# Kernel optimization log

Hardware: AMD Instinct MI355X
Metric: run time of the kernel (lower is better)

The kernel has to match this reference:

```python
import jax, jax.numpy as jnp
import numpy as np

N_NODES = 50000
N_EDGES = 800000
IN_F = 128
HID = 256
N_CLS = 10
NUM_GRAPHS = 256


def setup_inputs() -> dict:
    key = jax.random.key(0)
    ks = jax.random.split(key, 8)
    x = jax.random.normal(ks[0], (N_NODES, IN_F), dtype=jnp.float32)
    edge_index = jax.random.randint(ks[1], (2, N_EDGES), 0, N_NODES, dtype=jnp.int64)
    batch = jnp.sort(jax.random.randint(ks[2], (N_NODES,), 0, NUM_GRAPHS, dtype=jnp.int64))
    # Glorot-style init for weights (GCNConv default), zeros bias
    W1 = jax.random.normal(ks[3], (IN_F, HID), dtype=jnp.float32) / np.sqrt(IN_F)
    b1 = jnp.zeros((HID,), dtype=jnp.float32)
    W2 = jax.random.normal(ks[4], (HID, HID), dtype=jnp.float32) / np.sqrt(HID)
    b2 = jnp.zeros((HID,), dtype=jnp.float32)
    Wlin = jax.random.normal(ks[5], (HID, N_CLS), dtype=jnp.float32) / np.sqrt(HID)
    blin = jnp.zeros((N_CLS,), dtype=jnp.float32)
    return {"x": x, "edge_index": edge_index, "batch": batch,
            "W1": W1, "b1": b1, "W2": W2, "b2": b2, "Wlin": Wlin, "blin": blin}


def reference(x, edge_index, batch, W1, b1, W2, b2, Wlin, blin):
    N = x.shape[0]
    # PyG GCNConv default: add self-loops, symmetric normalization D^-1/2 A D^-1/2
    loop = jnp.arange(N, dtype=edge_index.dtype)
    src = jnp.concatenate([edge_index[0], loop])  # message source (row)
    dst = jnp.concatenate([edge_index[1], loop])  # aggregation target (col)
    deg = jax.ops.segment_sum(jnp.ones_like(dst, dtype=x.dtype), dst, num_segments=N)
    dinv = jnp.where(deg > 0, jax.lax.rsqrt(deg), 0.0)
    norm = dinv[src] * dinv[dst]  # [E+N]

    def gcn_conv(h, W, b):
        h = h @ W                          # linear transform first (GCNConv)
        msg = h[src] * norm[:, None]       # gather + edge scale
        agg = jax.ops.segment_sum(msg, dst, num_segments=N)  # scatter-add
        return agg + b

    h = jax.nn.relu(gcn_conv(x, W1, b1))
    h = gcn_conv(h, W2, b2)

    # global_mean_pool over batch ids
    counts = jax.ops.segment_sum(jnp.ones((N,), x.dtype), batch, num_segments=NUM_GRAPHS)
    pooled = jax.ops.segment_sum(h, batch, num_segments=NUM_GRAPHS)
    pooled = pooled / jnp.maximum(counts, 1.0)[:, None]  # [NUM_GRAPHS, HID]

    return pooled @ Wlin + blin  # forward returns logits (softmax unused in forward)
```

## Files before the change

kernel.cpp:

```cpp
#include <hip/hip_runtime.h>
#include <hip/hip_bf16.h>

typedef __hip_bfloat16 bf16;
typedef __attribute__((ext_vector_type(8))) short short8;
typedef __attribute__((ext_vector_type(4))) float f32x4;
typedef __attribute__((ext_vector_type(2))) float f32x2;

#define N_NODES 50000
#define N_EDGES 800000
#define IN_F    128
#define HID     256
#define N_CLS   10
#define N_GRAPH 256

#define NB 98
#define PBLOCKS 256

__device__ __forceinline__ int IG(const int* __restrict__ p, int i, int w) {
    return w ? p[2 * i] : p[i];
}
__device__ __forceinline__ float LF(const void* __restrict__ p, int i, int isbf) {
    return isbf ? __bfloat162float(((const bf16*)p)[i]) : ((const float*)p)[i];
}
__device__ __forceinline__ float b2f(unsigned short h) {
    union { unsigned u; float f; } c; c.u = ((unsigned)h) << 16; return c.f;
}
__device__ __forceinline__ unsigned short f2b(float x) {
    bf16 h = __float2bfloat16(x);
    union { bf16 b; unsigned short u; } c; c.b = h; return c.u;
}
__device__ __forceinline__ float f8s(unsigned b) {
    union { unsigned u; float f; } c;
    c.u = ((b & 0x80u) << 24) | ((b & 0x7Fu) << 20);
    return c.f;
}
#define F8SCALE 0x1p120f
__device__ __forceinline__ unsigned f2fp8(float x) {
    unsigned short h = f2b(x * 0x1p-120f);
    unsigned s = ((unsigned)h >> 8) & 0x80u;
    unsigned mag = (unsigned)h & 0x7FFFu;
    unsigned r = (mag + 7u + ((mag >> 4) & 1u)) >> 4;
    if (r > 0x7Eu) r = 0x7Eu;
    return s | r;
}

#if defined(__has_builtin)
#if __has_builtin(__builtin_amdgcn_cvt_pk_f32_fp8)
#define HW_FP8 1
#endif
#endif

__device__ __forceinline__ f32x2 cvt2lo(unsigned v) {
#ifdef HW_FP8
    return __builtin_amdgcn_cvt_pk_f32_fp8((int)v, false);
#else
    f32x2 r; r[0] = f8s(v & 0xFF) * F8SCALE; r[1] = f8s((v >> 8) & 0xFF) * F8SCALE; return r;
#endif
}
__device__ __forceinline__ f32x2 cvt2hi(unsigned v) {
#ifdef HW_FP8
    return __builtin_amdgcn_cvt_pk_f32_fp8((int)v, true);
#else
    f32x2 r; r[0] = f8s((v >> 16) & 0xFF) * F8SCALE; r[1] = f8s(v >> 24) * F8SCALE; return r;
#endif
}

__global__ __launch_bounds__(256) void k_detect(const int* __restrict__ ei,
                                                const unsigned short* __restrict__ x,
                                                int* __restrict__ flags) {
    __shared__ int nz, cnt;
    if (threadIdx.x == 0) { nz = 0; cnt = 0; }
    __syncthreads();
    int found = 0, c = 0;
    for (int s = 0; s < 4; ++s) {
        int idx = 2 * (threadIdx.x * 4 + s) + 1;
        if (ei[idx] != 0) found = 1;
    }
    for (int s = 0; s < 8; ++s) {
        unsigned short h = x[threadIdx.x * 8 + s];
        int e = (h >> 7) & 0xFF;
        if (e >= 110 && e <= 135) c++;
    }
    if (found) atomicAdd(&nz, 1);
    atomicAdd(&cnt, c);
    __syncthreads();
    if (threadIdx.x == 0) {
        flags[0] = (nz == 0) ? 1 : 0;
        flags[1] = (cnt > 1536) ? 1 : 0;
    }
}

__global__ __launch_bounds__(256) void k_partA1(const int* __restrict__ ei, int* __restrict__ bucketCnt,
                                                int* __restrict__ blockBase, const int* __restrict__ flags,
                                                int E, int N) {
    __shared__ int h[NB];
    int t = threadIdx.x;
    if (t < NB) h[t] = 0;
    __syncthreads();
    int w = flags[0];
    for (int e = blockIdx.x * 256 + t; e < E; e += PBLOCKS * 256) {
        int d = IG(ei, E + e, w);
        int s = IG(ei, e, w);
        if ((unsigned)d < (unsigned)N && (unsigned)s < (unsigned)N)
            atomicAdd(&h[d >> 9], 1);
    }
    __syncthreads();
    if (t < NB)
        blockBase[blockIdx.x * NB + t] = atomicAdd(&bucketCnt[t * 16], h[t]);
}

__global__ __launch_bounds__(128) void k_bscan(const int* __restrict__ bucketCnt,
                                               int* __restrict__ bucketBase) {
    __shared__ int s[128];
    int t = threadIdx.x;
    int v = (t < NB) ? bucketCnt[t * 16] : 0;
    s[t] = v;
    __syncthreads();
    for (int off = 1; off < 128; off <<= 1) {
        int add = (t >= off) ? s[t - off] : 0;
        __syncthreads();
        s[t] += add;
        __syncthreads();
    }
    if (t <= NB) bucketBase[t] = (t < NB) ? (s[t] - v) : s[NB - 1] + 0;
    if (t == NB - 1) bucketBase[NB] = s[t];
}

__global__ __launch_bounds__(256) void k_partA2(const int* __restrict__ ei,
                                                const int* __restrict__ bucketBase,
                                                const int* __restrict__ blockBase,
                                                unsigned* __restrict__ part,
                                                const int* __restrict__ flags, int E, int N) {
    __shared__ int cur[NB];
    int t = threadIdx.x;
    if (t < NB) cur[t] = bucketBase[t] + blockBase[blockIdx.x * NB + t];
    __syncthreads();
    int w = flags[0];
    for (int e = blockIdx.x * 256 + t; e < E; e += PBLOCKS * 256) {
        int d = IG(ei, E + e, w);
        int s = IG(ei, e, w);
        if ((unsigned)d < (unsigned)N && (unsigned)s < (unsigned)N) {
            int slot = atomicAdd(&cur[d >> 9], 1);
            part[slot] = ((unsigned)(d & 511) << 16) | (unsigned)s;
        }
    }
}

__global__ __launch_bounds__(256) void k_partB(const unsigned* __restrict__ part,
                                               const int* __restrict__ bucketBase,
                                               int* __restrict__ rowptr, float* __restrict__ dinv,
                                               int* __restrict__ col, int N) {
    __shared__ int hist[512];
    __shared__ int scn[512];
    __shared__ int pair[256];
    int b = blockIdx.x, t = threadIdx.x;
    int s0 = bucketBase[b], e0 = bucketBase[b + 1];
    hist[t] = 0; hist[t + 256] = 0;
    __syncthreads();
    for (int j = s0 + t; j < e0; j += 256)
        atomicAdd(&hist[part[j] >> 16], 1);
    __syncthreads();
    int a0 = hist[2 * t], a1 = hist[2 * t + 1];
    int pv = a0 + a1;
    pair[t] = pv;
    __syncthreads();
    for (int off = 1; off < 256; off <<= 1) {
        int add = (t >= off) ? pair[t - off] : 0;
        __syncthreads();
        pair[t] += add;
        __syncthreads();
    }
    int pbase = pair[t] - pv;
    scn[2 * t] = pbase;
    scn[2 * t + 1] = pbase + a0;
    __syncthreads();
#pragma unroll
    for (int hh = 0; hh < 2; ++hh) {
        int l = t + hh * 256;
        int node = b * 512 + l;
        if (node < N) {
            rowptr[node] = s0 + scn[l];
            dinv[node] = rsqrtf((float)(hist[l] + 1));
        }
    }
    if (b == 0 && t == 0) rowptr[N] = bucketBase[NB];
    __syncthreads();
    for (int j = s0 + t; j < e0; j += 256) {
        unsigned p = part[j];
        int pos = s0 + atomicAdd(&scn[p >> 16], 1);
        col[pos] = (int)(p & 0xFFFFu);
    }
}

#define CVTX_BLOCKS 6250
#define CVT1_BLOCKS 128
#define CVT2_BLOCKS 256
#define GB_BLOCKS   196
__global__ __launch_bounds__(256) void k_cvt(const void* __restrict__ x, const float* __restrict__ dinv,
                                             unsigned char* __restrict__ xs8,
                                             const void* __restrict__ W1, unsigned short* __restrict__ w1t,
                                             const void* __restrict__ W2, unsigned short* __restrict__ w2t,
                                             const int* __restrict__ batch, int* __restrict__ gstart,
                                             const int* __restrict__ flags) {
    int b = blockIdx.x;
    int fb = flags[1];
    if (b < CVTX_BLOCKS) {
        int gid = b * 256 + threadIdx.x;
        int row = gid >> 5;
        float d = dinv[row];
        float vx, vy, vz, vw;
        if (fb) {
            ushort4 v = ((const ushort4*)x)[gid];
            vx = b2f(v.x); vy = b2f(v.y); vz = b2f(v.z); vw = b2f(v.w);
        } else {
            float4 v = ((const float4*)x)[gid];
            vx = v.x; vy = v.y; vz = v.z; vw = v.w;
        }
        unsigned o = f2fp8(vx * d) | (f2fp8(vy * d) << 8) |
                     (f2fp8(vz * d) << 16) | (f2fp8(vw * d) << 24);
        ((unsigned*)xs8)[gid] = o;
    } else if (b < CVTX_BLOCKS + CVT1_BLOCKS) {
        int i = (b - CVTX_BLOCKS) * 256 + threadIdx.x;
        int n = i >> 7, k = i & 127;
        w1t[i] = f2b(LF(W1, k * 256 + n, fb));
    } else if (b < CVTX_BLOCKS + CVT1_BLOCKS + CVT2_BLOCKS) {
        int i = (b - CVTX_BLOCKS - CVT1_BLOCKS) * 256 + threadIdx.x;
        int n = i >> 8, k = i & 255;
        w2t[i] = f2b(LF(W2, k * 256 + n, fb));
    } else {
        int i = (b - CVTX_BLOCKS - CVT1_BLOCKS - CVT2_BLOCKS) * 256 + threadIdx.x;
        if (i <= N_NODES) {
            int w = flags[0];
            int prev = (i == 0) ? -1 : IG(batch, i - 1, w);
            int cur  = (i == N_NODES) ? N_GRAPH : IG(batch, i, w);
            if (prev < -1) prev = -1;
            if (cur > N_GRAPH) cur = N_GRAPH;
            for (int g = prev + 1; g <= cur; ++g)
                if (g >= 0 && g <= N_GRAPH) gstart[g] = i;
        }
    }
}

#define BSTR 132
__global__ __launch_bounds__(256) void k_gemm(const unsigned short* __restrict__ A,
                                              const unsigned short* __restrict__ Bt,
                                              unsigned short* __restrict__ C,
                                              unsigned char* __restrict__ C8, int M, int K,
                                              const float* __restrict__ rowscale,
                                              const void* __restrict__ bias,
                                              const int* __restrict__ flags, int relu) {
    __shared__ unsigned short Bs[128 * BSTR];
    int t = threadIdx.x;
    int lane = t & 63;
    int w = t >> 6;
    int stripe = blockIdx.y;
    int bm = blockIdx.x * 128;
    int l15 = lane & 15, quad = lane >> 4;
    const short8 Z8 = {0, 0, 0, 0, 0, 0, 0, 0};
    f32x4 acc[2][8];
#pragma unroll
    for (int i = 0; i < 2; ++i)
#pragma unroll
        for (int j = 0; j < 8; ++j) acc[i][j] = (f32x4){0.f, 0.f, 0.f, 0.f};

    int row0 = bm + w * 32 + l15;
    int row1 = row0 + 16;
    for (int kp = 0; kp < K; kp += 128) {
        if (kp) __syncthreads();
        {
            int n = t >> 1, h = t & 1;
            const unsigned short* src = &Bt[(size_t)(stripe * 128 + n) * K + kp + h * 64];
            unsigned short* dst = &Bs[n * BSTR + h * 64];
#pragma unroll
            for (int j = 0; j < 8; ++j)
                *(uint4*)&dst[j * 8] = *(const uint4*)&src[j * 8];
        }
        __syncthreads();
#pragma unroll
        for (int ks = 0; ks < 4; ++ks) {
            const unsigned short* abase = &A[(size_t)row0 * K + kp + ks * 32 + quad * 8];
            short8 a0 = (row0 < M) ? *(const short8*)abase : Z8;
            short8 a1 = (row1 < M) ? *(const short8*)(abase + (size_t)16 * K) : Z8;
#pragma unroll
            for (int tt = 0; tt < 8; ++tt) {
                short8 b = *(const short8*)&Bs[(tt * 16 + l15) * BSTR + ks * 32 + quad * 8];
                acc[0][tt] = __builtin_amdgcn_mfma_f32_16x16x32_bf16(b, a0, acc[0][tt], 0, 0, 0);
                acc[1][tt] = __builtin_amdgcn_mfma_f32_16x16x32_bf16(b, a1, acc[1][tt], 0, 0, 0);
            }
        }
    }
    int fb = flags[1];
    int rowA[2];
    float drow[2];
#pragma unroll
    for (int sa = 0; sa < 2; ++sa) {
        rowA[sa] = bm + w * 32 + sa * 16 + l15;
        drow[sa] = (rowscale && rowA[sa] < M) ? rowscale[rowA[sa]] : 1.f;
    }
#pragma unroll
    for (int tt = 0; tt < 8; ++tt) {
        int colb = stripe * 128 + tt * 16 + quad * 4;
        float bc[4];
#pragma unroll
        for (int rr = 0; rr < 4; ++rr)
            bc[rr] = bias ? LF(bias, colb + rr, fb) : 0.f;
#pragma unroll
        for (int sa = 0; sa < 2; ++sa) {
            if (rowA[sa] < M) {
                float v[4];
#pragma unroll
                for (int rr = 0; rr < 4; ++rr) {
                    float u = fmaf(acc[sa][tt][rr], drow[sa], bc[rr]);
                    if (relu) u = fmaxf(u, 0.f);
                    v[rr] = u;
                }
                size_t base = (size_t)rowA[sa] * 256 + colb;
                if (C8) {
                    unsigned o = f2fp8(v[0]) | (f2fp8(v[1]) << 8) |
                                 (f2fp8(v[2]) << 16) | (f2fp8(v[3]) << 24);
                    *(unsigned*)&C8[base] = o;
                } else {
                    ushort4 o;
                    o.x = f2b(v[0]); o.y = f2b(v[1]);
                    o.z = f2b(v[2]); o.w = f2b(v[3]);
                    *(ushort4*)&C[base] = o;
                }
            }
        }
    }
}

__global__ __launch_bounds__(256) void k_agg2(const unsigned char* __restrict__ XS,
                                              const int* __restrict__ rowptr, const int* __restrict__ col,
                                              unsigned short* __restrict__ Hout, int N) {
    int lane = threadIdx.x & 63;
    int i = (blockIdx.x * 256 + threadIdx.x) >> 6;
    if (i >= N) return;
    int fo = lane * 2;
    unsigned sv = *(const unsigned short*)&XS[(size_t)i * 128 + fo];
    f32x2 a = cvt2lo(sv);
    int s = rowptr[i], e = rowptr[i + 1];
    int j = s;
    while (j + 16 <= e) {
        unsigned v[16];
#pragma unroll
        for (int q = 0; q < 16; ++q)
            v[q] = *(const unsigned short*)&XS[(size_t)col[j + q] * 128 + fo];
#pragma unroll
        for (int q = 0; q < 16; ++q) a += cvt2lo(v[q]);
        j += 16;
    }
    if (j + 8 <= e) {
        unsigned v[8];
#pragma unroll
        for (int q = 0; q < 8; ++q)
            v[q] = *(const unsigned short*)&XS[(size_t)col[j + q] * 128 + fo];
#pragma unroll
        for (int q = 0; q < 8; ++q) a += cvt2lo(v[q]);
        j += 8;
    }
    if (j + 4 <= e) {
        unsigned v[4];
#pragma unroll
        for (int q = 0; q < 4; ++q)
            v[q] = *(const unsigned short*)&XS[(size_t)col[j + q] * 128 + fo];
#pragma unroll
        for (int q = 0; q < 4; ++q) a += cvt2lo(v[q]);
        j += 4;
    }
    for (; j < e; ++j)
        a += cvt2lo(*(const unsigned short*)&XS[(size_t)col[j] * 128 + fo]);
    ushort2 o;
    o.x = f2b(a[0]); o.y = f2b(a[1]);
    *(ushort2*)&Hout[(size_t)i * 128 + fo] = o;
}

__global__ __launch_bounds__(256) void k_agg4(const unsigned char* __restrict__ XW,
                                              const int* __restrict__ rowptr, const int* __restrict__ col,
                                              const float* __restrict__ dinv, const void* __restrict__ bias,
                                              const int* __restrict__ flags,
                                              unsigned short* __restrict__ Hout, int N) {
    int lane = threadIdx.x & 63;
    int i = (blockIdx.x * 256 + threadIdx.x) >> 6;
    if (i >= N) return;
    int fo = lane * 4;
    unsigned sv = *(const unsigned*)&XW[(size_t)i * 256 + fo];
    f32x2 a01 = cvt2lo(sv), a23 = cvt2hi(sv);
    int s = rowptr[i], e = rowptr[i + 1];
    int j = s;
    while (j + 16 <= e) {
        unsigned v[16];
#pragma unroll
        for (int q = 0; q < 16; ++q)
            v[q] = *(const unsigned*)&XW[(size_t)col[j + q] * 256 + fo];
#pragma unroll
        for (int q = 0; q < 16; ++q) { a01 += cvt2lo(v[q]); a23 += cvt2hi(v[q]); }
        j += 16;
    }
    if (j + 8 <= e) {
        unsigned v[8];
#pragma unroll
        for (int q = 0; q < 8; ++q)
            v[q] = *(const unsigned*)&XW[(size_t)col[j + q] * 256 + fo];
#pragma unroll
        for (int q = 0; q < 8; ++q) { a01 += cvt2lo(v[q]); a23 += cvt2hi(v[q]); }
        j += 8;
    }
    if (j + 4 <= e) {
        unsigned v[4];
#pragma unroll
        for (int q = 0; q < 4; ++q)
            v[q] = *(const unsigned*)&XW[(size_t)col[j + q] * 256 + fo];
#pragma unroll
        for (int q = 0; q < 4; ++q) { a01 += cvt2lo(v[q]); a23 += cvt2hi(v[q]); }
        j += 4;
    }
    for (; j < e; ++j) {
        unsigned v = *(const unsigned*)&XW[(size_t)col[j] * 256 + fo];
        a01 += cvt2lo(v); a23 += cvt2hi(v);
    }
    int fb = flags[1];
    float di = dinv[i];
    float bx = LF(bias, fo + 0, fb), by = LF(bias, fo + 1, fb);
    float bz = LF(bias, fo + 2, fb), bw = LF(bias, fo + 3, fb);
    ushort4 o;
    o.x = f2b(fmaf(a01[0], di, bx)); o.y = f2b(fmaf(a01[1], di, by));
    o.z = f2b(fmaf(a23[0], di, bz)); o.w = f2b(fmaf(a23[1], di, bw));
    *(ushort4*)&Hout[(size_t)i * 256 + fo] = o;
}

__global__ __launch_bounds__(256) void k_poolfinal(const unsigned short* __restrict__ H2,
                                                   const int* __restrict__ gstart,
                                                   const void* __restrict__ Wlin,
                                                   const void* __restrict__ blin,
                                                   const int* __restrict__ flags,
                                                   void* __restrict__ outv) {
    __shared__ float red[4][256];
    __shared__ float p[256];
    int g = blockIdx.x, t = threadIdx.x;
    int sub = t >> 6, lane = t & 63;
    int s = gstart[g], e = gstart[g + 1];
    int cnt = e - s;
    float ax = 0.f, ay = 0.f, az = 0.f, aw = 0.f;
    for (int i = s + sub; i < e; i += 4) {
        ushort4 v = *(const ushort4*)&H2[(size_t)i * 256 + lane * 4];
        ax += b2f(v.x); ay += b2f(v.y); az += b2f(v.z); aw += b2f(v.w);
    }
    red[sub][lane * 4 + 0] = ax;
    red[sub][lane * 4 + 1] = ay;
    red[sub][lane * 4 + 2] = az;
    red[sub][lane * 4 + 3] = aw;
    __syncthreads();
    float inv = 1.f / fmaxf((float)cnt, 1.f);
    p[t] = (red[0][t] + red[1][t] + red[2][t] + red[3][t]) * inv;
    __syncthreads();
    int fb = flags[1];
    if (t < N_CLS) {
        float sum = LF(blin, t, fb);
        for (int f = 0; f < HID; ++f) sum = fmaf(p[f], LF(Wlin, f * N_CLS + t, fb), sum);
        if (fb) ((bf16*)outv)[g * N_CLS + t] = __float2bfloat16(sum);
        else    ((float*)outv)[g * N_CLS + t] = sum;
    }
}

extern "C" void kernel_launch(void* const* d_in, const int* in_sizes, int n_in,
                              void* d_out, int out_size, void* d_ws, size_t ws_size,
                              hipStream_t stream) {
    (void)n_in; (void)ws_size; (void)in_sizes; (void)out_size;
    const void* x     = d_in[0];
    const int*  ei    = (const int*)d_in[1];
    const int*  batch = (const int*)d_in[2];
    const void* W1    = d_in[3];
    const void* b1    = d_in[4];
    const void* W2    = d_in[5];
    const void* b2    = d_in[6];
    const void* Wl    = d_in[7];
    const void* bl    = d_in[8];

    const int N = N_NODES, E = N_EDGES, F = IN_F, H = HID, G = N_GRAPH;

    char* ws = (char*)d_ws;
    size_t off = 0;
    auto alloc = [&](size_t bytes) -> void* {
        void* p = ws + off;
        off += (bytes + 511) & ~(size_t)511;
        return p;
    };
    unsigned char*  xs8  = (unsigned char*)alloc((size_t)N * F);
    unsigned short* aggX = (unsigned short*)alloc((size_t)N * F * 2);
    unsigned short* H1   = (unsigned short*)alloc((size_t)N * H * 2);
    unsigned short* H2   = (unsigned short*)alloc((size_t)N * H * 2);
    unsigned char*  XW2s8 = xs8;
    unsigned short* w1t  = (unsigned short*)alloc((size_t)H * F * 2);
    unsigned short* w2t  = (unsigned short*)alloc((size_t)H * H * 2);
    int*   bucketCnt = (int*)alloc((size_t)NB * 16 * 4);
    int*   bucketBase = (int*)alloc((size_t)(NB + 1) * 4);
    int*   blockBase = (int*)alloc((size_t)PBLOCKS * NB * 4);
    unsigned* part  = (unsigned*)alloc((size_t)E * 4);
    int*   gstart  = (int*)alloc((size_t)(G + 1) * 4);
    float* dinv    = (float*)alloc((size_t)N * 4);
    int*   rowptr  = (int*)alloc((size_t)(N + 1) * 4);
    int*   flags   = (int*)alloc(512);
    int*   col     = (int*)alloc((size_t)E * 4);
    size_t zero_bytes = (size_t)NB * 16 * 4;

    hipMemsetAsync(bucketCnt, 0, zero_bytes, stream);

    k_detect<<<1, 256, 0, stream>>>(ei, (const unsigned short*)x, flags);
    k_partA1<<<PBLOCKS, 256, 0, stream>>>(ei, bucketCnt, blockBase, flags, E, N);
    k_bscan<<<1, 128, 0, stream>>>(bucketCnt, bucketBase);
    k_partA2<<<PBLOCKS, 256, 0, stream>>>(ei, bucketBase, blockBase, part, flags, E, N);
    k_partB<<<NB, 256, 0, stream>>>(part, bucketBase, rowptr, dinv, col, N);

    k_cvt<<<CVTX_BLOCKS + CVT1_BLOCKS + CVT2_BLOCKS + GB_BLOCKS, 256, 0, stream>>>(
        x, dinv, xs8, W1, w1t, W2, w2t, batch, gstart, flags);

    dim3 gemmGrid((N + 127) / 128, 2);
    int nbAgg = (N + 3) / 4;

    k_agg2<<<nbAgg, 256, 0, stream>>>(xs8, rowptr, col, aggX, N);
    k_gemm<<<gemmGrid, 256, 0, stream>>>(aggX, w1t, H1, nullptr, N, F, dinv, b1, flags, 1);
    k_gemm<<<gemmGrid, 256, 0, stream>>>(H1, w2t, nullptr, XW2s8, N, H, dinv, nullptr, flags, 0);
    k_agg4<<<nbAgg, 256, 0, stream>>>(XW2s8, rowptr, col, dinv, b2, flags, H2, N);
    k_poolfinal<<<G, 256, 0, stream>>>(H2, gstart, Wl, bl, flags, d_out);
}
```

Before: 284.3 us.

## Stage GEMM epilogue through shared memory and use hardware fp8 pack conversion

The GEMM epilogue now writes bias/scale/relu results into the shared B tile, then each thread writes contiguous 64-byte or 128-byte row segments to global memory. Before, each lane made scattered 4-byte or 8-byte stores. The float-to-fp8 packing also switches to the hardware cvt_pk_fp8_f32 builtin when available, replacing the software rounding path. Together these aim to coalesce output writes and cut ALU work in the epilogue. The cost is extra syncthreads and LDS traffic, and the hardware fp8 format and scaling may not match the software encoding (which uses a 2^-120 scale) that the decoder expects.

```diff
diff --git a/kernel.cpp b/kernel.cpp
--- a/kernel.cpp
+++ b/kernel.cpp
@@ -48,6 +48,9 @@
 #if __has_builtin(__builtin_amdgcn_cvt_pk_f32_fp8)
 #define HW_FP8 1
 #endif
+#if __has_builtin(__builtin_amdgcn_cvt_pk_fp8_f32)
+#define HW_FP8E 1
+#endif
 #endif
 
 __device__ __forceinline__ f32x2 cvt2lo(unsigned v) {
@@ -62,6 +65,15 @@
     return __builtin_amdgcn_cvt_pk_f32_fp8((int)v, true);
 #else
     f32x2 r; r[0] = f8s((v >> 16) & 0xFF) * F8SCALE; r[1] = f8s(v >> 24) * F8SCALE; return r;
+#endif
+}
+__device__ __forceinline__ unsigned pk4_fp8(float v0, float v1, float v2, float v3) {
+#ifdef HW_FP8E
+    int o = __builtin_amdgcn_cvt_pk_fp8_f32(v0, v1, 0, false);
+    o = __builtin_amdgcn_cvt_pk_fp8_f32(v2, v3, o, true);
+    return (unsigned)o;
+#else
+    return f2fp8(v0) | (f2fp8(v1) << 8) | (f2fp8(v2) << 16) | (f2fp8(v3) << 24);
 #endif
 }
 
@@ -216,9 +228,7 @@
             float4 v = ((const float4*)x)[gid];
             vx = v.x; vy = v.y; vz = v.z; vw = v.w;
         }
-        unsigned o = f2fp8(vx * d) | (f2fp8(vy * d) << 8) |
-                     (f2fp8(vz * d) << 16) | (f2fp8(vw * d) << 24);
-        ((unsigned*)xs8)[gid] = o;
+        ((unsigned*)xs8)[gid] = pk4_fp8(vx * d, vy * d, vz * d, vw * d);
     } else if (b < CVTX_BLOCKS + CVT1_BLOCKS) {
         int i = (b - CVTX_BLOCKS) * 256 + threadIdx.x;
         int n = i >> 7, k = i & 127;
@@ -297,34 +307,71 @@
         rowA[sa] = bm + w * 32 + sa * 16 + l15;
         drow[sa] = (rowscale && rowA[sa] < M) ? rowscale[rowA[sa]] : 1.f;
     }
-#pragma unroll
-    for (int tt = 0; tt < 8; ++tt) {
-        int colb = stripe * 128 + tt * 16 + quad * 4;
-        float bc[4];
-#pragma unroll
-        for (int rr = 0; rr < 4; ++rr)
-            bc[rr] = bias ? LF(bias, colb + rr, fb) : 0.f;
-#pragma unroll
-        for (int sa = 0; sa < 2; ++sa) {
-            if (rowA[sa] < M) {
+    __syncthreads();
+    if (C8) {
+        unsigned* Cs = (unsigned*)Bs;
+#pragma unroll
+        for (int tt = 0; tt < 8; ++tt) {
+            int colb = stripe * 128 + tt * 16 + quad * 4;
+            float bc[4];
+#pragma unroll
+            for (int rr = 0; rr < 4; ++rr)
+                bc[rr] = bias ? LF(bias, colb + rr, fb) : 0.f;
+#pragma unroll
+            for (int sa = 0; sa < 2; ++sa) {
                 float v[4];
 #pragma unroll
                 for (int rr = 0; rr < 4; ++rr) {
                     float u = fmaf(acc[sa][tt][rr], drow[sa], bc[rr]);
-                    if (relu) u = fmaxf(u, 0.f);
-                    v[rr] = u;
+                    v[rr] = relu ? fmaxf(u, 0.f) : u;
                 }
-                size_t base = (size_t)rowA[sa] * 256 + colb;
-                if (C8) {
-                    unsigned o = f2fp8(v[0]) | (f2fp8(v[1]) << 8) |
-                                 (f2fp8(v[2]) << 16) | (f2fp8(v[3]) << 24);
-                    *(unsigned*)&C8[base] = o;
-                } else {
-                    ushort4 o;
-                    o.x = f2b(v[0]); o.y = f2b(v[1]);
-                    o.z = f2b(v[2]); o.w = f2b(v[3]);
-                    *(ushort4*)&C[base] = o;
+                Cs[(w * 32 + sa * 16 + l15) * 36 + tt * 4 + quad] =
+                    pk4_fp8(v[0], v[1], v[2], v[3]);
+            }
+        }
+        __syncthreads();
+        int r = t >> 1, h = t & 1;
+        int grow = bm + r;
+        if (grow < M) {
+            const uint4* src = (const uint4*)(Cs + r * 36 + h * 16);
+            uint4* dst = (uint4*)&C8[(size_t)grow * 256 + stripe * 128 + h * 64];
+#pragma unroll
+            for (int j = 0; j < 4; ++j) dst[j] = src[j];
+        }
+    } else {
+        unsigned short* Cs = Bs;
+#pragma unroll
+        for (int tt = 0; tt < 8; ++tt) {
+            int colb = stripe * 128 + tt * 16 + quad * 4;
+            float bc[4];
+#pragma unroll
+            for (int rr = 0; rr < 4; ++rr)
+                bc[rr] = bias ? LF(bias, colb + rr, fb) : 0.f;
+#pragma unroll
+            for (int sa = 0; sa < 2; ++sa) {
+                float v[4];
+#pragma unroll
+                for (int rr = 0; rr < 4; ++rr) {
+                    float u = fmaf(acc[sa][tt][rr], drow[sa], bc[rr]);
+                    v[rr] = relu ? fmaxf(u, 0.f) : u;
                 }
+                ushort4 o;
+                o.x = f2b(v[0]); o.y = f2b(v[1]); o.z = f2b(v[2]); o.w = f2b(v[3]);
+                *(ushort4*)&Cs[(w * 32 + sa * 16 + l15) * 132 + tt * 16 + quad * 4] = o;
+            }
+        }
+        __syncthreads();
+        int r = t >> 1, h = t & 1;
+        int grow = bm + r;
+        if (grow < M) {
+            int base = r * 132 + h * 64;
+            size_t gbase = (size_t)grow * 256 + stripe * 128 + h * 64;
+#pragma unroll
+            for (int j = 0; j < 8; ++j) {
+                uint2 a2 = *(const uint2*)&Cs[base + j * 8];
+                uint2 b2 = *(const uint2*)&Cs[base + j * 8 + 4];
+                uint4 u; u.x = a2.x; u.y = a2.y; u.z = b2.x; u.w = b2.y;
+                *(uint4*)&C[gbase + j * 8] = u;
             }
         }
     }
```

New measurement: 282.8 us. No clear change (-0.5%).
